# Kernel optimization log

Measured on AMD Instinct MI355X. Metric: run time of the kernel, lower is better.

Reference implementation:

```python
import jax, jax.numpy as jnp
import numpy as np

GAMMA = 0.99  # discount_factor
RHO = 1.0     # rho truncation level
CIS = 1.0     # cis truncation level
T, B = 2048, 8192  # (seq_len, batch)


def setup_inputs() -> dict:
    key = jax.random.key(0)
    k1, k2, k3, k4 = jax.random.split(key, 4)
    return {
        "target_value": jax.random.normal(k1, (T, B), jnp.float32),
        "rewards": jax.random.normal(k2, (T, B), jnp.float32),
        "target_log_policy": jax.random.normal(k3, (T, B), jnp.float32) * 0.1,
        "behaviour_log_policy": jax.random.normal(k4, (T, B), jnp.float32) * 0.1,
    }


def reference(target_value, rewards, target_log_policy, behaviour_log_policy):
    # importance sampling weights, truncated
    is_w = jnp.exp(target_log_policy - behaviour_log_policy)
    rhos = jnp.minimum(RHO, is_w)   # (T, B)
    ciss = jnp.minimum(CIS, is_w)   # (T, B)

    v = target_value
    v_next = v[1:]                  # V(x_{s+1}), (T-1, B)
    # delta_s = rho_s * (r_s + gamma*V(x_{s+1}) - V(x_s))
    delta = rhos[:-1] * (rewards[:-1] + GAMMA * v_next - v[:-1])
    # vtrace_s = a_s + b_s * vtrace_{s+1}, affine recurrence coefficients:
    a = v[:-1] + delta - GAMMA * ciss[:-1] * v_next  # (T-1, B)
    b = GAMMA * ciss[:-1]                             # (T-1, B)

    def step(carry, ab):
        a_i, b_i = ab
        vt = a_i + b_i * carry
        return vt, vt

    last = v[-1]  # vtrace[-1] = V(x_{T-1})
    _, vs = jax.lax.scan(step, last, (a, b), reverse=True)  # (T-1, B)
    vtrace = jnp.concatenate([vs, last[None]], axis=0)      # (T, B)
    return vtrace, rhos
```

## Files before the change

kernel.cpp:

```cpp
#include <hip/hip_runtime.h>

#define T_DIM 2048
#define B_DIM 8192
#define GAMMA 0.99f
#define NCHUNK 256
#define CHUNK_L (T_DIM / NCHUNK)

__global__ __launch_bounds__(256) void vtrace_pass1(
    const float* __restrict__ v, const float* __restrict__ rew,
    const float* __restrict__ tlp, const float* __restrict__ blp,
    float* __restrict__ out_a,
    float* __restrict__ out_rho,
    float* __restrict__ Aw, float* __restrict__ Bw)
{
    const int j   = blockIdx.x * blockDim.x + threadIdx.x;
    const int c   = blockIdx.y;
    const int col = j * 4;
    const int t_hi = (c + 1) * CHUNK_L - 1;
    const int t_lo = c * CHUNK_L;

    float4 A  = make_float4(0.f, 0.f, 0.f, 0.f);
    float4 Bc = make_float4(1.f, 1.f, 1.f, 1.f);

    int idx = t_hi * B_DIM + col;
    #pragma unroll
    for (int t = t_hi; t >= t_lo; --t, idx -= B_DIM) {
        const float4 v4 = *(const float4*)(v   + idx);
        const float4 r4 = *(const float4*)(rew + idx);
        const float4 t4 = *(const float4*)(tlp + idx);
        const float4 b4 = *(const float4*)(blp + idx);

        float4 rho;
        rho.x = fminf(1.f, __expf(t4.x - b4.x));
        rho.y = fminf(1.f, __expf(t4.y - b4.y));
        rho.z = fminf(1.f, __expf(t4.z - b4.z));
        rho.w = fminf(1.f, __expf(t4.w - b4.w));
        *(float4*)(out_rho + idx) = rho;

        float4 a4, bv;
        if (t == T_DIM - 1) {
            a4 = v4;
            bv = make_float4(0.f, 0.f, 0.f, 0.f);
        } else {
            a4.x = fmaf(rho.x, r4.x - v4.x, v4.x);
            a4.y = fmaf(rho.y, r4.y - v4.y, v4.y);
            a4.z = fmaf(rho.z, r4.z - v4.z, v4.z);
            a4.w = fmaf(rho.w, r4.w - v4.w, v4.w);
            bv.x = GAMMA * rho.x;
            bv.y = GAMMA * rho.y;
            bv.z = GAMMA * rho.z;
            bv.w = GAMMA * rho.w;
        }
        *(float4*)(out_a + idx) = a4;

        A.x = fmaf(bv.x, A.x, a4.x);
        A.y = fmaf(bv.y, A.y, a4.y);
        A.z = fmaf(bv.z, A.z, a4.z);
        A.w = fmaf(bv.w, A.w, a4.w);
        Bc.x *= bv.x; Bc.y *= bv.y; Bc.z *= bv.z; Bc.w *= bv.w;
    }

    const int widx = c * B_DIM + col;
    *(float4*)(Aw + widx) = A;
    *(float4*)(Bw + widx) = Bc;
}

__global__ __launch_bounds__(256) void vtrace_carry(
    const float* __restrict__ Aw, const float* __restrict__ Bw,
    float* __restrict__ cb)
{
    const int j = blockIdx.x * blockDim.x + threadIdx.x;
    float x = 0.f;
    #pragma unroll 8
    for (int c = NCHUNK - 1; c >= 0; --c) {
        const int i = c * B_DIM + j;
        const float Av = Aw[i];
        const float Bv = Bw[i];
        cb[i] = x;
        x = fmaf(Bv, x, Av);
    }
}

__global__ __launch_bounds__(256) void vtrace_pass2(
    float* __restrict__ out_v,
    const float* __restrict__ rho_arr,
    const float* __restrict__ cb)
{
    const int j   = blockIdx.x * blockDim.x + threadIdx.x;
    const int c   = blockIdx.y;
    const int col = j * 4;
    const int t_hi = (c + 1) * CHUNK_L - 1;
    const int t_lo = c * CHUNK_L;

    float4 carry = *(const float4*)(cb + c * B_DIM + col);

    int idx = t_hi * B_DIM + col;
    #pragma unroll
    for (int t = t_hi; t >= t_lo; --t, idx -= B_DIM) {
        const float4 a4  = *(const float4*)(out_v  + idx);
        const float4 rho = *(const float4*)(rho_arr + idx);
        const float g = (t == T_DIM - 1) ? 0.f : GAMMA;
        float4 o;
        o.x = fmaf(g * rho.x, carry.x, a4.x);
        o.y = fmaf(g * rho.y, carry.y, a4.y);
        o.z = fmaf(g * rho.z, carry.z, a4.z);
        o.w = fmaf(g * rho.w, carry.w, a4.w);
        *(float4*)(out_v + idx) = o;
        carry = o;
    }
}

extern "C" void kernel_launch(void* const* d_in, const int* in_sizes, int n_in,
                              void* d_out, int out_size, void* d_ws, size_t ws_size,
                              hipStream_t stream) {
    const float* v   = (const float*)d_in[0];
    const float* rew = (const float*)d_in[1];
    const float* tlp = (const float*)d_in[2];
    const float* blp = (const float*)d_in[3];

    float* out_v   = (float*)d_out;
    float* out_rho = out_v + (size_t)T_DIM * B_DIM;

    float* Aw = (float*)d_ws;
    float* Bw = Aw + (size_t)NCHUNK * B_DIM;
    float* cb = Bw + (size_t)NCHUNK * B_DIM;

    dim3 blk(256);
    dim3 grid_main(B_DIM / 4 / 256, NCHUNK);

    vtrace_pass1<<<grid_main, blk, 0, stream>>>(v, rew, tlp, blp,
                                                out_v, out_rho, Aw, Bw);
    vtrace_carry<<<dim3(B_DIM / 256), blk, 0, stream>>>(Aw, Bw, cb);
    vtrace_pass2<<<grid_main, blk, 0, stream>>>(out_v, out_rho, cb);
}
```

Baseline: 126.4 us.

## Split first pass into elementwise kernel and separate chunk-compose scan kernel

Moves the exp/rho and affine coefficient computation into a flat grid-stride elementwise kernel. A new kernel then re-reads the stored a and rho arrays to compose per-chunk affine summaries. The intent is better coalesced streaming for the heavy elementwise part. The cost is an extra full pass reading two large arrays and an additional kernel launch.

```diff
diff --git a/kernel.cpp b/kernel.cpp
--- a/kernel.cpp
+++ b/kernel.cpp
@@ -6,11 +6,45 @@
 #define NCHUNK 256
 #define CHUNK_L (T_DIM / NCHUNK)
 
-__global__ __launch_bounds__(256) void vtrace_pass1(
-    const float* __restrict__ v, const float* __restrict__ rew,
-    const float* __restrict__ tlp, const float* __restrict__ blp,
-    float* __restrict__ out_a,
-    float* __restrict__ out_rho,
+__global__ __launch_bounds__(256) void vtrace_elem(
+    const float4* __restrict__ v, const float4* __restrict__ rew,
+    const float4* __restrict__ tlp, const float4* __restrict__ blp,
+    float4* __restrict__ out_a, float4* __restrict__ out_rho)
+{
+    const int tid  = blockIdx.x * 256 + threadIdx.x;
+    const int NT   = 2048 * 256;
+    const int LAST = (T_DIM - 1) * (B_DIM / 4);
+
+    #pragma unroll
+    for (int k = 0; k < 8; ++k) {
+        const int i = tid + k * NT;
+        const float4 t4 = tlp[i];
+        const float4 b4 = blp[i];
+        const float4 v4 = v[i];
+        const float4 r4 = rew[i];
+
+        float4 rho;
+        rho.x = fminf(1.f, __expf(t4.x - b4.x));
+        rho.y = fminf(1.f, __expf(t4.y - b4.y));
+        rho.z = fminf(1.f, __expf(t4.z - b4.z));
+        rho.w = fminf(1.f, __expf(t4.w - b4.w));
+        out_rho[i] = rho;
+
+        float4 a4;
+        if (i >= LAST) {
+            a4 = v4;
+        } else {
+            a4.x = fmaf(rho.x, r4.x - v4.x, v4.x);
+            a4.y = fmaf(rho.y, r4.y - v4.y, v4.y);
+            a4.z = fmaf(rho.z, r4.z - v4.z, v4.z);
+            a4.w = fmaf(rho.w, r4.w - v4.w, v4.w);
+        }
+        out_a[i] = a4;
+    }
+}
+
+__global__ __launch_bounds__(256) void vtrace_comp(
+    const float* __restrict__ a_arr, const float* __restrict__ rho_arr,
     float* __restrict__ Aw, float* __restrict__ Bw)
 {
     const int j   = blockIdx.x * blockDim.x + threadIdx.x;
@@ -25,34 +59,10 @@
     int idx = t_hi * B_DIM + col;
     #pragma unroll
     for (int t = t_hi; t >= t_lo; --t, idx -= B_DIM) {
-        const float4 v4 = *(const float4*)(v   + idx);
-        const float4 r4 = *(const float4*)(rew + idx);
-        const float4 t4 = *(const float4*)(tlp + idx);
-        const float4 b4 = *(const float4*)(blp + idx);
-
-        float4 rho;
-        rho.x = fminf(1.f, __expf(t4.x - b4.x));
-        rho.y = fminf(1.f, __expf(t4.y - b4.y));
-        rho.z = fminf(1.f, __expf(t4.z - b4.z));
-        rho.w = fminf(1.f, __expf(t4.w - b4.w));
-        *(float4*)(out_rho + idx) = rho;
-
-        float4 a4, bv;
-        if (t == T_DIM - 1) {
-            a4 = v4;
-            bv = make_float4(0.f, 0.f, 0.f, 0.f);
-        } else {
-            a4.x = fmaf(rho.x, r4.x - v4.x, v4.x);
-            a4.y = fmaf(rho.y, r4.y - v4.y, v4.y);
-            a4.z = fmaf(rho.z, r4.z - v4.z, v4.z);
-            a4.w = fmaf(rho.w, r4.w - v4.w, v4.w);
-            bv.x = GAMMA * rho.x;
-            bv.y = GAMMA * rho.y;
-            bv.z = GAMMA * rho.z;
-            bv.w = GAMMA * rho.w;
-        }
-        *(float4*)(out_a + idx) = a4;
-
+        const float4 a4  = *(const float4*)(a_arr  + idx);
+        const float4 rho = *(const float4*)(rho_arr + idx);
+        const float g = (t == T_DIM - 1) ? 0.f : GAMMA;
+        const float4 bv = make_float4(g * rho.x, g * rho.y, g * rho.z, g * rho.w);
         A.x = fmaf(bv.x, A.x, a4.x);
         A.y = fmaf(bv.y, A.y, a4.y);
         A.z = fmaf(bv.z, A.z, a4.z);
@@ -81,7 +91,7 @@
     }
 }
 
-__global__ __launch_bounds__(256) void vtrace_pass2(
+__global__ __launch_bounds__(256) void vtrace_apply(
     float* __restrict__ out_v,
     const float* __restrict__ rho_arr,
     const float* __restrict__ cb)
@@ -97,7 +107,7 @@
     int idx = t_hi * B_DIM + col;
     #pragma unroll
     for (int t = t_hi; t >= t_lo; --t, idx -= B_DIM) {
-        const float4 a4  = *(const float4*)(out_v  + idx);
+        const float4 a4  = *(const float4*)(out_v   + idx);
         const float4 rho = *(const float4*)(rho_arr + idx);
         const float g = (t == T_DIM - 1) ? 0.f : GAMMA;
         float4 o;
@@ -126,10 +136,14 @@
     float* cb = Bw + (size_t)NCHUNK * B_DIM;
 
     dim3 blk(256);
-    dim3 grid_main(B_DIM / 4 / 256, NCHUNK);
 
-    vtrace_pass1<<<grid_main, blk, 0, stream>>>(v, rew, tlp, blp,
-                                                out_v, out_rho, Aw, Bw);
+    vtrace_elem<<<dim3(2048), blk, 0, stream>>>(
+        (const float4*)v, (const float4*)rew,
+        (const float4*)tlp, (const float4*)blp,
+        (float4*)out_v, (float4*)out_rho);
+
+    dim3 grid_scan(B_DIM / 4 / 256, NCHUNK);
+    vtrace_comp<<<grid_scan, blk, 0, stream>>>(out_v, out_rho, Aw, Bw);
     vtrace_carry<<<dim3(B_DIM / 256), blk, 0, stream>>>(Aw, Bw, cb);
-    vtrace_pass2<<<grid_main, blk, 0, stream>>>(out_v, out_rho, cb);
+    vtrace_apply<<<grid_scan, blk, 0, stream>>>(out_v, out_rho, cb);
 }
```

New measurement: 145.0 us. +14.7%, slower.
